# Kernel optimization log

Hardware: AMD Instinct MI355X
Metric: run time of the kernel (lower is better)

The kernel has to match this reference:

```python
import jax, jax.numpy as jnp
import numpy as np

N_NODES = 100000
N_EDGES = 1000000
D_IN = 64
D_H = 64
D_Z = 32
EPS = 1e-5          # BatchNorm1d default eps
NEG_SLOPE = 0.01    # nn.LeakyReLU default


def setup_inputs() -> dict:
    key = jax.random.key(0)
    ks = jax.random.split(key, 12)
    inp = {
        "x": jax.random.normal(ks[0], (N_NODES, D_IN), dtype=jnp.float32),
        "edge_index": jax.random.randint(ks[1], (2, N_EDGES), 0, N_NODES, dtype=jnp.int64),
        "edge_weight": jax.random.uniform(ks[2], (N_EDGES,), dtype=jnp.float32),
        "batch": jnp.zeros((N_NODES,), dtype=jnp.int64),
        # layer 1: D_IN -> D_H, with BatchNorm1d affine params
        "W1": jax.random.normal(ks[3], (D_IN, D_H), dtype=jnp.float32) / np.sqrt(D_IN),
        "b1": jnp.zeros((D_H,), dtype=jnp.float32),
        "g1": jnp.ones((D_H,), dtype=jnp.float32),
        "be1": jnp.zeros((D_H,), dtype=jnp.float32),
        # layer 2: D_H -> D_H
        "W2": jax.random.normal(ks[4], (D_H, D_H), dtype=jnp.float32) / np.sqrt(D_H),
        "b2": jnp.zeros((D_H,), dtype=jnp.float32),
        "g2": jnp.ones((D_H,), dtype=jnp.float32),
        "be2": jnp.zeros((D_H,), dtype=jnp.float32),
        # layer 3 (output): D_H -> D_Z, no norm/activation
        "W3": jax.random.normal(ks[5], (D_H, D_Z), dtype=jnp.float32) / np.sqrt(D_H),
        "b3": jnp.zeros((D_Z,), dtype=jnp.float32),
    }
    return inp


def _propagate(h, src, dst, w):
    # weighted message passing: gather source features, scale by edge weight,
    # scatter-add into destination nodes.  [E, d] intermediate.
    msgs = h[src] * w[:, None]
    return jax.ops.segment_sum(msgs, dst, num_segments=N_NODES)


def _batchnorm(h, gamma, beta):
    # BatchNorm1d in training mode: batch statistics over the node axis.
    mean = jnp.mean(h, axis=0)
    var = jnp.var(h, axis=0)
    return (h - mean) * jax.lax.rsqrt(var + EPS) * gamma + beta


def _leaky_relu(h):
    return jnp.where(h >= 0, h, NEG_SLOPE * h)


def reference(x, edge_index, edge_weight, batch, W1, b1, g1, be1, W2, b2, g2, be2, W3, b3):
    src, dst = edge_index[0], edge_index[1]
    # layer 1: GCN conv (aggregate -> linear) + BN + LeakyReLU (dropout=0 -> identity)
    h = _propagate(x, src, dst, edge_weight) @ W1 + b1
    h = _leaky_relu(_batchnorm(h, g1, be1))
    # layer 2
    h = _propagate(h, src, dst, edge_weight) @ W2 + b2
    h = _leaky_relu(_batchnorm(h, g2, be2))
    # output layer to z_dim, no norm / activation
    h = _propagate(h, src, dst, edge_weight) @ W3 + b3
    return h
```

## Files before the change

### kernel.cpp

```cpp
#include <hip/hip_runtime.h>
#include <math.h>

#define NEG_SLOPE 0.01f
#define NBLK 256
#define BND  256
#define STB  512

__device__ __forceinline__ unsigned short f2b(float f) {
    unsigned int u = __float_as_uint(f);
    u += 0x7FFFu + ((u >> 16) & 1u);
    return (unsigned short)(u >> 16);
}


__global__ void partA1(const int* __restrict__ dst, int* __restrict__ cmat,
                       int E, int epb, int nbk) {
    __shared__ int cnt[512];
    for (int i = threadIdx.x; i < 512; i += 512) cnt[i] = 0;
    __syncthreads();
    int b = blockIdx.x;
    int e0 = b * epb, e1 = min(e0 + epb, E);
    for (int e = e0 + threadIdx.x; e < e1; e += 512)
        atomicAdd(&cnt[dst[e] >> 8], 1);
    __syncthreads();
    for (int k = threadIdx.x; k < nbk; k += 512)
        cmat[k * NBLK + b] = cnt[k];
}

__global__ void scan_bsum(const int* __restrict__ in, int* __restrict__ bsums, int n) {
    int t = threadIdx.x;
    int i0 = blockIdx.x * 1024 + t * 4;
    int4 c;
    if (i0 + 3 < n) {
        c = *reinterpret_cast<const int4*>(in + i0);
    } else {
        c.x = (i0 + 0 < n) ? in[i0 + 0] : 0;
        c.y = (i0 + 1 < n) ? in[i0 + 1] : 0;
        c.z = (i0 + 2 < n) ? in[i0 + 2] : 0;
        c.w = (i0 + 3 < n) ? in[i0 + 3] : 0;
    }
    int s = c.x + c.y + c.z + c.w;
#pragma unroll
    for (int d = 32; d > 0; d >>= 1) s += __shfl_down(s, d);
    __shared__ int wtot[4];
    if ((t & 63) == 0) wtot[t >> 6] = s;
    __syncthreads();
    if (t == 0) bsums[blockIdx.x] = wtot[0] + wtot[1] + wtot[2] + wtot[3];
}

__global__ void scan_bsums(int* __restrict__ bsums, int* __restrict__ outx, int nb, int n) {
    __shared__ int lds[128];
    int t = threadIdx.x;
    int v = (t < nb) ? bsums[t] : 0;
    lds[t] = v;
    __syncthreads();
    for (int d = 1; d < 128; d <<= 1) {
        int u = (t >= d) ? lds[t - d] : 0;
        __syncthreads();
        lds[t] += u;
        __syncthreads();
    }
    if (t < nb) bsums[t] = lds[t] - v;
    if (t == 127) outx[n] = lds[127];
}

__global__ void scan_excl(const int* __restrict__ in, const int* __restrict__ bbase,
                          int* __restrict__ outx, int n) {
    int t = threadIdx.x;
    int lane = t & 63, wid = t >> 6;
    int i0 = blockIdx.x * 1024 + t * 4;
    int4 c;
    if (i0 + 3 < n) {
        c = *reinterpret_cast<const int4*>(in + i0);
    } else {
        c.x = (i0 + 0 < n) ? in[i0 + 0] : 0;
        c.y = (i0 + 1 < n) ? in[i0 + 1] : 0;
        c.z = (i0 + 2 < n) ? in[i0 + 2] : 0;
        c.w = (i0 + 3 < n) ? in[i0 + 3] : 0;
    }
    int s = c.x + c.y + c.z + c.w;
    int inc = s;
#pragma unroll
    for (int d = 1; d < 64; d <<= 1) {
        int v = __shfl_up(inc, d);
        if (lane >= d) inc += v;
    }
    __shared__ int wtot[4];
    if (lane == 63) wtot[wid] = inc;
    __syncthreads();
    int wbase = 0;
    for (int i = 0; i < wid; ++i) wbase += wtot[i];
    int excl = bbase[blockIdx.x] + wbase + inc - s;
    int o0 = excl, o1 = o0 + c.x, o2 = o1 + c.y, o3 = o2 + c.z;
    if (i0 + 3 < n) {
        *reinterpret_cast<int4*>(outx + i0) = make_int4(o0, o1, o2, o3);
    } else {
        if (i0 + 0 < n) outx[i0 + 0] = o0;
        if (i0 + 1 < n) outx[i0 + 1] = o1;
        if (i0 + 2 < n) outx[i0 + 2] = o2;
        if (i0 + 3 < n) outx[i0 + 3] = o3;
    }
}

__global__ void partA2(const int* __restrict__ src, const int* __restrict__ dst,
                       const float* __restrict__ w, const int* __restrict__ cbase,
                       int2* __restrict__ binned, int E, int epb, int nbk) {
    __shared__ int cur[512];
    int b = blockIdx.x;
    for (int k = threadIdx.x; k < nbk; k += 512) cur[k] = cbase[k * NBLK + b];
    __syncthreads();
    int e0 = b * epb, e1 = min(e0 + epb, E);
    for (int e = e0 + threadIdx.x; e < e1; e += 512) {
        int d = dst[e];
        int pos = atomicAdd(&cur[d >> 8], 1);
        binned[pos] = make_int2(__float_as_int(w[e]), src[e] | ((d & 255) << 18));
    }
}

__global__ void partB(const int* __restrict__ cbase, const int2* __restrict__ binned,
                      int2* __restrict__ csr8, int* __restrict__ offsets,
                      int N, int E, int nbk) {
    __shared__ int lcnt[256], lofs[256];
    int b = blockIdx.x;
    int t = threadIdx.x;
    lcnt[t] = 0;
    __syncthreads();
    int bstart = cbase[b * NBLK];
    int bend   = cbase[(b + 1) * NBLK];
    for (int i = bstart + t; i < bend; i += 256)
        atomicAdd(&lcnt[(binned[i].y >> 18) & 255], 1);
    __syncthreads();
    int v = lcnt[t];
    lofs[t] = v;
    __syncthreads();
    for (int d = 1; d < 256; d <<= 1) {
        int u = (t >= d) ? lofs[t - d] : 0;
        __syncthreads();
        lofs[t] += u;
        __syncthreads();
    }
    int excl = lofs[t] - v;
    int node = (b << 8) + t;
    if (node < N) offsets[node] = bstart + excl;
    if (b == nbk - 1 && t == 0) offsets[N] = E;
    __syncthreads();
    lcnt[t] = bstart + excl;
    __syncthreads();
    for (int i = bstart + t; i < bend; i += 256) {
        int2 r = binned[i];
        int pos = atomicAdd(&lcnt[(r.y >> 18) & 255], 1);
        csr8[pos] = make_int2(r.y & 0x3FFFF, r.x);
    }
}


template <int LPR, bool F32OUT>
__global__ __launch_bounds__(256, 8) void prop_kernel(
        const uint4* __restrict__ in4, const int* __restrict__ offsets,
        const int2* __restrict__ csr8, const float* __restrict__ bias,
        void* __restrict__ outv, int n) {
    constexpr int NG = 64 / LPR;
    int wave = (blockIdx.x * 256 + threadIdx.x) >> 6;
    int lane = threadIdx.x & 63;
    int g    = lane / LPR;
    int c    = lane % LPR;
    int row  = wave * NG + g;
    bool valid = row < n;
    int start = 0, end = 0;
    if (valid) { start = offsets[row]; end = offsets[row + 1]; }
    float4 accA = make_float4(0.f, 0.f, 0.f, 0.f);
    float4 accB = make_float4(0.f, 0.f, 0.f, 0.f);
    int i = start;
    int rem = end - start;
    while (__any(rem > 0)) {
        int2  rec[4];
        uint4 dat[4];
#pragma unroll
        for (int j = 0; j < 4; ++j) {
            if (j < rem) rec[j] = csr8[i + j];
        }
#pragma unroll
        for (int j = 0; j < 4; ++j) {
            if (j < rem) dat[j] = in4[(size_t)rec[j].x * LPR + c];
        }
#pragma unroll
        for (int j = 0; j < 4; ++j) {
            if (j < rem) {
                float w = __int_as_float(rec[j].y);
                accA.x = fmaf(__uint_as_float(dat[j].x << 16),         w, accA.x);
                accA.y = fmaf(__uint_as_float(dat[j].x & 0xFFFF0000u), w, accA.y);
                accA.z = fmaf(__uint_as_float(dat[j].y << 16),         w, accA.z);
                accA.w = fmaf(__uint_as_float(dat[j].y & 0xFFFF0000u), w, accA.w);
                accB.x = fmaf(__uint_as_float(dat[j].z << 16),         w, accB.x);
                accB.y = fmaf(__uint_as_float(dat[j].z & 0xFFFF0000u), w, accB.y);
                accB.z = fmaf(__uint_as_float(dat[j].w << 16),         w, accB.z);
                accB.w = fmaf(__uint_as_float(dat[j].w & 0xFFFF0000u), w, accB.w);
            }
        }
        i   += 4;
        rem -= 4;
    }
    if (valid) {
        const float4* b4 = reinterpret_cast<const float4*>(bias);
        float4 ba = b4[c * 2], bb = b4[c * 2 + 1];
        accA.x += ba.x; accA.y += ba.y; accA.z += ba.z; accA.w += ba.w;
        accB.x += bb.x; accB.y += bb.y; accB.z += bb.z; accB.w += bb.w;
        if (F32OUT) {
            float4* o = reinterpret_cast<float4*>(outv) + (size_t)row * LPR * 2;
            o[c * 2]     = accA;
            o[c * 2 + 1] = accB;
        } else {
            uint4 o;
            o.x = (unsigned int)f2b(accA.x) | ((unsigned int)f2b(accA.y) << 16);
            o.y = (unsigned int)f2b(accA.z) | ((unsigned int)f2b(accA.w) << 16);
            o.z = (unsigned int)f2b(accB.x) | ((unsigned int)f2b(accB.y) << 16);
            o.w = (unsigned int)f2b(accB.z) | ((unsigned int)f2b(accB.w) << 16);
            reinterpret_cast<uint4*>(outv)[(size_t)row * LPR + c] = o;
        }
    }
}


__global__ void gemm1_kernel(const float* __restrict__ A, const float* __restrict__ W,
                             unsigned short* __restrict__ out, int n) {
    __shared__ float Wl[64 * 64];
    for (int i = threadIdx.x; i < 64 * 64; i += 256) Wl[i] = W[i];
    __syncthreads();
    int rl = threadIdx.x >> 4;
    int c4 = threadIdx.x & 15;
    int row = blockIdx.x * 16 + rl;
    if (row >= n) return;
    const float4* Ar = reinterpret_cast<const float4*>(A + (size_t)row * 64);
    float4 acc = make_float4(0.f, 0.f, 0.f, 0.f);
#pragma unroll
    for (int k4 = 0; k4 < 16; ++k4) {
        float4 a4 = Ar[k4];
#pragma unroll
        for (int j = 0; j < 4; ++j) {
            float a = (&a4.x)[j];
            const float* wp = &Wl[(k4 * 4 + j) * 64 + c4 * 4];
            acc.x = fmaf(a, wp[0], acc.x);
            acc.y = fmaf(a, wp[1], acc.y);
            acc.z = fmaf(a, wp[2], acc.z);
            acc.w = fmaf(a, wp[3], acc.w);
        }
    }
    unsigned int lo = (unsigned int)f2b(acc.x) | ((unsigned int)f2b(acc.y) << 16);
    unsigned int hi = (unsigned int)f2b(acc.z) | ((unsigned int)f2b(acc.w) << 16);
    reinterpret_cast<uint2*>(out + (size_t)row * 64)[c4] = make_uint2(lo, hi);
}


template <int DOUT>
__global__ void gemm_bn(const unsigned short* __restrict__ A, const float* __restrict__ W,
                        const float* __restrict__ ss, unsigned short* __restrict__ out, int n) {
    constexpr int C4  = DOUT / 4;
    constexpr int RPB = 256 / C4;
    __shared__ float Wl[64 * DOUT];
    __shared__ float scl[64], shl[64];
    for (int i = threadIdx.x; i < 64 * DOUT; i += 256) Wl[i] = W[i];
    if (threadIdx.x < 64)       scl[threadIdx.x] = ss[threadIdx.x];
    else if (threadIdx.x < 128) shl[threadIdx.x - 64] = ss[threadIdx.x];
    __syncthreads();
    int rl = threadIdx.x / C4;
    int c4 = threadIdx.x % C4;
    int row = blockIdx.x * RPB + rl;
    if (row >= n) return;
    const uint2* Ar = reinterpret_cast<const uint2*>(A + (size_t)row * 64);
    float4 acc = make_float4(0.f, 0.f, 0.f, 0.f);
#pragma unroll
    for (int k4 = 0; k4 < 16; ++k4) {
        uint2 a2 = Ar[k4];
        float f[4];
        f[0] = __uint_as_float(a2.x << 16);
        f[1] = __uint_as_float(a2.x & 0xFFFF0000u);
        f[2] = __uint_as_float(a2.y << 16);
        f[3] = __uint_as_float(a2.y & 0xFFFF0000u);
#pragma unroll
        for (int j = 0; j < 4; ++j) {
            int kk = k4 * 4 + j;
            float v = fmaf(f[j], scl[kk], shl[kk]);
            v = (v >= 0.f) ? v : NEG_SLOPE * v;
            const float* wp = &Wl[kk * DOUT + c4 * 4];
            acc.x = fmaf(v, wp[0], acc.x);
            acc.y = fmaf(v, wp[1], acc.y);
            acc.z = fmaf(v, wp[2], acc.z);
            acc.w = fmaf(v, wp[3], acc.w);
        }
    }
    unsigned int lo = (unsigned int)f2b(acc.x) | ((unsigned int)f2b(acc.y) << 16);
    unsigned int hi = (unsigned int)f2b(acc.z) | ((unsigned int)f2b(acc.w) << 16);
    reinterpret_cast<uint2*>(out + (size_t)row * DOUT)[c4] = make_uint2(lo, hi);
}


__global__ void stats_kernel(const unsigned int* __restrict__ hu, float* __restrict__ part, int n) {
    int t  = threadIdx.x;
    int rg = t >> 5;
    int dw = t & 31;
    float s0 = 0.f, s1 = 0.f, q0 = 0.f, q1 = 0.f;
    for (int r = blockIdx.x * 8 + rg; r < n; r += gridDim.x * 8) {
        unsigned int u = hu[(size_t)r * 32 + dw];
        float v0 = __uint_as_float(u << 16);
        float v1 = __uint_as_float(u & 0xFFFF0000u);
        s0 += v0; q0 += v0 * v0;
        s1 += v1; q1 += v1 * v1;
    }
    __shared__ float ls[8][64], lq[8][64];
    ls[rg][2 * dw]     = s0; lq[rg][2 * dw]     = q0;
    ls[rg][2 * dw + 1] = s1; lq[rg][2 * dw + 1] = q1;
    __syncthreads();
    if (t < 64) {
        float a = 0.f;
        for (int r = 0; r < 8; ++r) a += ls[r][t];
        part[blockIdx.x * 128 + t] = a;
    } else if (t < 128) {
        float a = 0.f;
        for (int r = 0; r < 8; ++r) a += lq[r][t - 64];
        part[blockIdx.x * 128 + t] = a;
    }
}


__global__ void redpart_kernel(const float* __restrict__ part, double* __restrict__ red, int nb) {
    int b = blockIdx.x;
    double acc = 0.0;
    for (int i = threadIdx.x; i < nb; i += 256)
        acc += (double)part[(size_t)i * 128 + b];
#pragma unroll
    for (int d = 32; d > 0; d >>= 1) acc += __shfl_down(acc, d);
    __shared__ double wv[4];
    if ((threadIdx.x & 63) == 0) wv[threadIdx.x >> 6] = acc;
    __syncthreads();
    if (threadIdx.x == 0) red[b] = wv[0] + wv[1] + wv[2] + wv[3];
}

__global__ void bnfin_small(const double* __restrict__ red, const float* __restrict__ g,
                            const float* __restrict__ be, float* __restrict__ ss, int n) {
    int t = threadIdx.x;
    if (t < 64) {
        double mean = red[t] / n;
        double var  = red[64 + t] / n - mean * mean;
        double inv  = 1.0 / sqrt(var + 1e-5);
        float scale = (float)(inv * (double)g[t]);
        ss[t]      = scale;
        ss[64 + t] = be[t] - (float)mean * scale;
    }
}


extern "C" void kernel_launch(void* const* d_in, const int* in_sizes, int n_in,
                              void* d_out, int out_size, void* d_ws, size_t ws_size,
                              hipStream_t stream) {
    const float* x    = (const float*)d_in[0];
    const int*   ei   = (const int*)d_in[1];
    const float* ew   = (const float*)d_in[2];
    const float* W1   = (const float*)d_in[4];
    const float* b1   = (const float*)d_in[5];
    const float* g1p  = (const float*)d_in[6];
    const float* be1  = (const float*)d_in[7];
    const float* W2   = (const float*)d_in[8];
    const float* b2   = (const float*)d_in[9];
    const float* g2p  = (const float*)d_in[10];
    const float* be2  = (const float*)d_in[11];
    const float* W3   = (const float*)d_in[12];
    const float* b3   = (const float*)d_in[13];
    float* out = (float*)d_out;

    const int N = in_sizes[0] / 64;
    const int E = in_sizes[2];
    const int* src = ei;
    const int* dst = ei + E;

    const int nbk = (N + BND - 1) / BND;
    const int M   = nbk * NBLK;
    const int epb = (E + NBLK - 1) / NBLK;

    char* wsb = (char*)d_ws;
    size_t off = 0;
    auto alloc = [&](size_t bytes) -> void* {
        off = (off + 255) & ~(size_t)255;
        void* p = wsb + off;
        off += bytes;
        return p;
    };
    unsigned short* g   = (unsigned short*)alloc((size_t)N * 64 * 2);
    unsigned short* h   = (unsigned short*)alloc((size_t)N * 64 * 2);
    unsigned short* g3  = (unsigned short*)alloc((size_t)N * 32 * 2);
    int2*   csr8    = (int2*)alloc((size_t)E * 8);
    int*    cmat    = (int*)alloc((size_t)M * 4);
    int*    cbase   = (int*)alloc((size_t)(M + 1) * 4);
    int*    offsets = (int*)alloc((size_t)(N + 1) * 4);
    int*    bsums   = (int*)alloc(1024 * 4);
    float*  part    = (float*)alloc((size_t)STB * 128 * 4);
    double* red1    = (double*)alloc(128 * 8);
    double* red2    = (double*)alloc(128 * 8);
    float*  ss1     = (float*)alloc(128 * 4);
    float*  ss2     = (float*)alloc(128 * 4);
    int2*   binned  = (int2*)g;
    (void)ws_size; (void)n_in; (void)out_size;

    const int waves64 = (N + 7) / 8;
    const int pb64    = (waves64 * 64 + 255) / 256;
    const int waves32 = (N + 15) / 16;
    const int pb32    = (waves32 * 64 + 255) / 256;
    const int gb16    = (N + 15) / 16;
    const int gb32    = (N + 31) / 32;
    const int nbM     = (M + 1023) / 1024;

    partA1<<<NBLK, 512, 0, stream>>>(dst, cmat, E, epb, nbk);
    scan_bsum<<<nbM, 256, 0, stream>>>(cmat, bsums, M);
    scan_bsums<<<1, 128, 0, stream>>>(bsums, cbase, nbM, M);
    scan_excl<<<nbM, 256, 0, stream>>>(cmat, bsums, cbase, M);
    partA2<<<NBLK, 512, 0, stream>>>(src, dst, ew, cbase, binned, E, epb, nbk);
    partB<<<nbk, 256, 0, stream>>>(cbase, binned, csr8, offsets, N, E, nbk);

    gemm1_kernel<<<gb16, 256, 0, stream>>>(x, W1, g, N);
    prop_kernel<8, false><<<pb64, 256, 0, stream>>>((const uint4*)g, offsets, csr8, b1, h, N);
    stats_kernel<<<STB, 256, 0, stream>>>((const unsigned int*)h, part, N);
    redpart_kernel<<<128, 256, 0, stream>>>(part, red1, STB);
    bnfin_small<<<1, 64, 0, stream>>>(red1, g1p, be1, ss1, N);

    gemm_bn<64><<<gb16, 256, 0, stream>>>(h, W2, ss1, g, N);
    prop_kernel<8, false><<<pb64, 256, 0, stream>>>((const uint4*)g, offsets, csr8, b2, h, N);
    stats_kernel<<<STB, 256, 0, stream>>>((const unsigned int*)h, part, N);
    redpart_kernel<<<128, 256, 0, stream>>>(part, red2, STB);
    bnfin_small<<<1, 64, 0, stream>>>(red2, g2p, be2, ss2, N);

    gemm_bn<32><<<gb32, 256, 0, stream>>>(h, W3, ss2, g3, N);
    prop_kernel<4, true><<<pb32, 256, 0, stream>>>((const uint4*)g3, offsets, csr8, b3, out, N);
}
```

Measured before the change: 204.7 us.

## Sort nodes by degree to balance per-wave work in propagation

Builds a degree histogram and counting-sort permutation of nodes after CSR construction, and makes each propagation wave process rows taken from this permutation. Grouping rows of similar degree is meant to reduce idle lanes when the wave loops until its longest row finishes. It adds five small kernels per call, an extra indirection load, and scattered output row writes that lose contiguity.

Result: slower. 220.2 us (+7.6%).

```diff
diff --git a/kernel.cpp b/kernel.cpp
--- a/kernel.cpp
+++ b/kernel.cpp
@@ -5,6 +5,7 @@
 #define NBLK 256
 #define BND  256
 #define STB  512
+#define DBLK 128
 
 __device__ __forceinline__ unsigned short f2b(float f) {
     unsigned int u = __float_as_uint(f);
@@ -154,20 +155,53 @@
 }
 
 
+__global__ void dhist(const int* __restrict__ offsets, int* __restrict__ dmat, int N, int rpb) {
+    __shared__ int cnt[64];
+    int b = blockIdx.x;
+    if (threadIdx.x < 64) cnt[threadIdx.x] = 0;
+    __syncthreads();
+    int r0 = b * rpb, r1 = min(r0 + rpb, N);
+    for (int r = r0 + threadIdx.x; r < r1; r += 256) {
+        int deg = min(offsets[r + 1] - offsets[r], 63);
+        atomicAdd(&cnt[deg], 1);
+    }
+    __syncthreads();
+    if (threadIdx.x < 64) dmat[threadIdx.x * DBLK + b] = cnt[threadIdx.x];
+}
+
+__global__ void dscatter(const int* __restrict__ offsets, const int* __restrict__ dbase,
+                         int* __restrict__ perm, int N, int rpb) {
+    __shared__ int cur[64];
+    int b = blockIdx.x;
+    if (threadIdx.x < 64) cur[threadIdx.x] = dbase[threadIdx.x * DBLK + b];
+    __syncthreads();
+    int r0 = b * rpb, r1 = min(r0 + rpb, N);
+    for (int r = r0 + threadIdx.x; r < r1; r += 256) {
+        int deg = min(offsets[r + 1] - offsets[r], 63);
+        int pos = atomicAdd(&cur[deg], 1);
+        perm[pos] = r;
+    }
+}
+
+
 template <int LPR, bool F32OUT>
 __global__ __launch_bounds__(256, 8) void prop_kernel(
         const uint4* __restrict__ in4, const int* __restrict__ offsets,
-        const int2* __restrict__ csr8, const float* __restrict__ bias,
-        void* __restrict__ outv, int n) {
+        const int2* __restrict__ csr8, const int* __restrict__ perm,
+        const float* __restrict__ bias, void* __restrict__ outv, int n) {
     constexpr int NG = 64 / LPR;
     int wave = (blockIdx.x * 256 + threadIdx.x) >> 6;
     int lane = threadIdx.x & 63;
     int g    = lane / LPR;
     int c    = lane % LPR;
-    int row  = wave * NG + g;
-    bool valid = row < n;
-    int start = 0, end = 0;
-    if (valid) { start = offsets[row]; end = offsets[row + 1]; }
+    int idx  = wave * NG + g;
+    bool valid = idx < n;
+    int row = 0, start = 0, end = 0;
+    if (valid) {
+        row   = perm[idx];
+        start = offsets[row];
+        end   = offsets[row + 1];
+    }
     float4 accA = make_float4(0.f, 0.f, 0.f, 0.f);
     float4 accB = make_float4(0.f, 0.f, 0.f, 0.f);
     int i = start;
@@ -375,6 +409,8 @@
     const int nbk = (N + BND - 1) / BND;
     const int M   = nbk * NBLK;
     const int epb = (E + NBLK - 1) / NBLK;
+    const int Md  = 64 * DBLK;
+    const int rpbd = (N + DBLK - 1) / DBLK;
 
     char* wsb = (char*)d_ws;
     size_t off = 0;
@@ -392,6 +428,9 @@
     int*    cbase   = (int*)alloc((size_t)(M + 1) * 4);
     int*    offsets = (int*)alloc((size_t)(N + 1) * 4);
     int*    bsums   = (int*)alloc(1024 * 4);
+    int*    dmat    = (int*)alloc((size_t)Md * 4);
+    int*    dbase   = (int*)alloc((size_t)(Md + 1) * 4);
+    int*    perm    = (int*)alloc((size_t)N * 4);
     float*  part    = (float*)alloc((size_t)STB * 128 * 4);
     double* red1    = (double*)alloc(128 * 8);
     double* red2    = (double*)alloc(128 * 8);
@@ -407,6 +446,7 @@
     const int gb16    = (N + 15) / 16;
     const int gb32    = (N + 31) / 32;
     const int nbM     = (M + 1023) / 1024;
+    const int nbMd    = (Md + 1023) / 1024;
 
     partA1<<<NBLK, 512, 0, stream>>>(dst, cmat, E, epb, nbk);
     scan_bsum<<<nbM, 256, 0, stream>>>(cmat, bsums, M);
@@ -415,18 +455,24 @@
     partA2<<<NBLK, 512, 0, stream>>>(src, dst, ew, cbase, binned, E, epb, nbk);
     partB<<<nbk, 256, 0, stream>>>(cbase, binned, csr8, offsets, N, E, nbk);
 
+    dhist<<<DBLK, 256, 0, stream>>>(offsets, dmat, N, rpbd);
+    scan_bsum<<<nbMd, 256, 0, stream>>>(dmat, bsums, Md);
+    scan_bsums<<<1, 128, 0, stream>>>(bsums, dbase, nbMd, Md);
+    scan_excl<<<nbMd, 256, 0, stream>>>(dmat, bsums, dbase, Md);
+    dscatter<<<DBLK, 256, 0, stream>>>(offsets, dbase, perm, N, rpbd);
+
     gemm1_kernel<<<gb16, 256, 0, stream>>>(x, W1, g, N);
-    prop_kernel<8, false><<<pb64, 256, 0, stream>>>((const uint4*)g, offsets, csr8, b1, h, N);
+    prop_kernel<8, false><<<pb64, 256, 0, stream>>>((const uint4*)g, offsets, csr8, perm, b1, h, N);
     stats_kernel<<<STB, 256, 0, stream>>>((const unsigned int*)h, part, N);
     redpart_kernel<<<128, 256, 0, stream>>>(part, red1, STB);
     bnfin_small<<<1, 64, 0, stream>>>(red1, g1p, be1, ss1, N);
 
     gemm_bn<64><<<gb16, 256, 0, stream>>>(h, W2, ss1, g, N);
-    prop_kernel<8, false><<<pb64, 256, 0, stream>>>((const uint4*)g, offsets, csr8, b2, h, N);
+    prop_kernel<8, false><<<pb64, 256, 0, stream>>>((const uint4*)g, offsets, csr8, perm, b2, h, N);
     stats_kernel<<<STB, 256, 0, stream>>>((const unsigned int*)h, part, N);
     redpart_kernel<<<128, 256, 0, stream>>>(part, red2, STB);
     bnfin_small<<<1, 64, 0, stream>>>(red2, g2p, be2, ss2, N);
 
     gemm_bn<32><<<gb32, 256, 0, stream>>>(h, W3, ss2, g3, N);
-    prop_kernel<4, true><<<pb32, 256, 0, stream>>>((const uint4*)g3, offsets, csr8, b3, out, N);
-}
+    prop_kernel<4, true><<<pb32, 256, 0, stream>>>((const uint4*)g3, offsets, csr8, perm, b3, out, N);
+}
```
